# Performance work log

Hardware: AMD Instinct MI355X
Metric: run time of the kernel (lower is better)

Reference implementation:

```python
import jax, jax.numpy as jnp
import numpy as np

MARGIN = 0.3


def _pairwise_dist(x):
    # Exact euclidean cdist; same math as torch.cdist's non-mm mode:
    # sqrt(sum_k (x_i[k]-x_j[k])^2) == sqrt(|x_i|^2 + |x_j|^2 - 2 x_i.x_j).
    sq = jnp.sum(x * x, axis=1)
    sqd = sq[:, None] + sq[None, :] - 2.0 * (x @ x.T)
    sqd = jnp.maximum(sqd, 0.0)
    # safe sqrt: zero distance (diagonal) -> dist 0 with zero grad, like torch
    safe = jnp.where(sqd > 0, sqd, 1.0)
    return jnp.where(sqd > 0, jnp.sqrt(safe), 0.0)


def setup_inputs() -> dict:
    key = jax.random.key(0)
    k1, k2 = jax.random.split(key)
    n, d, n_classes = 8192, 128, 64
    inputs = jax.random.normal(k1, (n, d), dtype=jnp.float32)
    targets = jax.random.randint(k2, (n,), 0, n_classes)
    return {"inputs": inputs, "targets": targets}


def reference(inputs, targets):
    dist = _pairwise_dist(inputs)  # (n, n)
    mask = targets[:, None] == targets[None, :]  # (n, n) same-label mask
    # hard positive: max distance among same-label (diag included, as in torch code)
    dist_ap = jnp.max(jnp.where(mask, dist, -jnp.inf), axis=1)  # (n,)
    # hard negative: min distance among different-label
    dist_an = jnp.min(jnp.where(mask, jnp.inf, dist), axis=1)  # (n,)
    # MarginRankingLoss with y=1: mean(relu(-(dist_an - dist_ap) + margin))
    loss = jnp.mean(jax.nn.relu(dist_ap - dist_an + MARGIN))
    return (loss, dist)
```

## Files before the change

kernel.cpp:

```cpp
#include <hip/hip_runtime.h>
#include <hip/hip_bf16.h>
#include <cstdint>
#include <cstddef>


#define NROWS 8192
#define DIMK  128
#define MARGIN 0.3f

typedef __bf16 bf16x8 __attribute__((ext_vector_type(8)));
typedef float  f32x4  __attribute__((ext_vector_type(4)));
typedef int    i32x4  __attribute__((ext_vector_type(4)));
typedef float  f32x2  __attribute__((ext_vector_type(2)));

__device__ __forceinline__ unsigned short f2bf(float f) {
    unsigned u = __float_as_uint(f);
    u += 0x7fffu + ((u >> 16) & 1u);
    return (unsigned short)(u >> 16);
}

__global__ __launch_bounds__(256) void prep_kernel(
    const float* __restrict__ X, unsigned short* __restrict__ Xb,
    float* __restrict__ sq, int* __restrict__ ap, int* __restrict__ an)
{
    const int t = blockIdx.x * 256 + threadIdx.x;
    if (t < NROWS) { ap[t] = 0; an[t] = 0x7f800000; }
    const int row  = t >> 6;
    const int lane = t & 63;
    const f32x2 v = *(const f32x2*)(X + (size_t)row * DIMK + lane * 2);
    const unsigned short b0 = f2bf(v[0]);
    const unsigned short b1 = f2bf(v[1]);
    *(unsigned*)(Xb + (size_t)row * DIMK + lane * 2) =
        (unsigned)b0 | ((unsigned)b1 << 16);
    const float f0 = __uint_as_float((unsigned)b0 << 16);
    const float f1 = __uint_as_float((unsigned)b1 << 16);
    float s = f0 * f0 + f1 * f1;
    #pragma unroll
    for (int off = 32; off; off >>= 1) s += __shfl_xor(s, off);
    if (lane == 0) sq[row] = s;
}

__global__ __launch_bounds__(256, 2) void dist_kernel(
    const unsigned short* __restrict__ Xb, const float* __restrict__ sq,
    const int* __restrict__ tgt, float* __restrict__ dist,
    int* __restrict__ ap, int* __restrict__ an)
{
    __shared__ unsigned short As[128 * DIMK];
    __shared__ unsigned short Bs[128 * DIMK];

    const int t  = threadIdx.x;
    const int bm = blockIdx.x, bn = blockIdx.y;

    {
        const char* gA = (const char*)Xb + (size_t)bm * (128 * DIMK * 2);
        const char* gB = (const char*)Xb + (size_t)bn * (128 * DIMK * 2);
        #pragma unroll
        for (int i = 0; i < 8; i++) {
            const int off = i * 4096 + t * 16;
            __builtin_amdgcn_global_load_lds(
                (const __attribute__((address_space(1))) void*)(gA + off),
                (__attribute__((address_space(3))) void*)((char*)As + off),
                16, 0, 0);
        }
        #pragma unroll
        for (int i = 0; i < 8; i++) {
            const int off = i * 4096 + t * 16;
            __builtin_amdgcn_global_load_lds(
                (const __attribute__((address_space(1))) void*)(gB + off),
                (__attribute__((address_space(3))) void*)((char*)Bs + off),
                16, 0, 0);
        }
    }
    __syncthreads();

    const int lane = t & 63, wave = t >> 6;
    const int wm = (wave >> 1) * 64, wn = (wave & 1) * 64;
    const int l15 = lane & 15, quad = lane >> 4;

    f32x4 acc[4][4];
    #pragma unroll
    for (int mi = 0; mi < 4; mi++)
        #pragma unroll
        for (int ni = 0; ni < 4; ni++)
            acc[mi][ni] = (f32x4){0.f, 0.f, 0.f, 0.f};

    #pragma unroll
    for (int ks = 0; ks < 4; ks++) {
        const int kb = ks * 32 + quad * 8;
        bf16x8 a_frag[4], b_frag[4];
        #pragma unroll
        for (int mi = 0; mi < 4; mi++)
            a_frag[mi] = *(const bf16x8*)(As + (wm + mi * 16 + l15) * DIMK + kb);
        #pragma unroll
        for (int ni = 0; ni < 4; ni++)
            b_frag[ni] = *(const bf16x8*)(Bs + (wn + ni * 16 + l15) * DIMK + kb);
        #pragma unroll
        for (int mi = 0; mi < 4; mi++)
            #pragma unroll
            for (int ni = 0; ni < 4; ni++)
                acc[mi][ni] = __builtin_amdgcn_mfma_f32_16x16x32_bf16(
                    a_frag[mi], b_frag[ni], acc[mi][ni], 0, 0, 0);
    }

    const int rbase = bm * 128 + wm;
    const int cbase = bn * 128 + wn;
    const float INF = __int_as_float(0x7f800000);

    float sqc[4]; int tc[4]; int cg[4];
    #pragma unroll
    for (int ni = 0; ni < 4; ni++) {
        cg[ni]  = cbase + ni * 16 + l15;
        sqc[ni] = sq[cg[ni]];
        tc[ni]  = tgt[cg[ni]];
    }

    #pragma unroll
    for (int mi = 0; mi < 4; mi++) {
        const int rg0 = rbase + mi * 16 + quad * 4;
        const f32x4 sqr = *(const f32x4*)(sq + rg0);
        const i32x4 tr  = *(const i32x4*)(tgt + rg0);
        #pragma unroll
        for (int reg = 0; reg < 4; reg++) {
            const int rg = rg0 + reg;
            float apv = -1.0f, anv = INF;
            #pragma unroll
            for (int ni = 0; ni < 4; ni++) {
                const float dot = acc[mi][ni][reg];
                float sqd = sqr[reg] + sqc[ni] - 2.0f * dot;
                float d = sqd > 0.0f ? sqrtf(sqd) : 0.0f;
                if (rg == cg[ni]) d = 0.0f;
                __builtin_nontemporal_store(d, dist + (size_t)rg * NROWS + cg[ni]);
                const bool same = (tr[reg] == tc[ni]);
                apv = fmaxf(apv, same ? d : -1.0f);
                anv = fminf(anv, same ? INF : d);
            }
            #pragma unroll
            for (int m = 1; m < 16; m <<= 1) {
                apv = fmaxf(apv, __shfl_xor(apv, m));
                anv = fminf(anv, __shfl_xor(anv, m));
            }
            if (l15 == mi * 4 + reg) {
                atomicMax(ap + rg, __float_as_int(apv));
                atomicMin(an + rg, __float_as_int(anv));
            }
        }
    }
}

__global__ __launch_bounds__(256) void loss_kernel(
    const int* __restrict__ ap, const int* __restrict__ an,
    float* __restrict__ out)
{
    __shared__ float red[4];
    float s = 0.0f;
    for (int i = threadIdx.x; i < NROWS; i += 256) {
        const float v = __int_as_float(ap[i]) - __int_as_float(an[i]) + MARGIN;
        s += v > 0.0f ? v : 0.0f;
    }
    #pragma unroll
    for (int off = 32; off; off >>= 1) s += __shfl_xor(s, off);
    if ((threadIdx.x & 63) == 0) red[threadIdx.x >> 6] = s;
    __syncthreads();
    if (threadIdx.x == 0)
        out[0] = (red[0] + red[1] + red[2] + red[3]) * (1.0f / NROWS);
}

extern "C" void kernel_launch(void* const* d_in, const int* in_sizes, int n_in,
                              void* d_out, int out_size, void* d_ws, size_t ws_size,
                              hipStream_t stream)
{
    const float* X   = (const float*)d_in[0];
    const int*   tgt = (const int*)d_in[1];
    float*       out = (float*)d_out;

    unsigned short* Xb = (unsigned short*)d_ws;
    float* sq = (float*)((char*)d_ws + (size_t)NROWS * DIMK * 2);
    int*   ap = (int*)(sq + NROWS);
    int*   an = ap + NROWS;

    prep_kernel<<<(NROWS * 64) / 256, 256, 0, stream>>>(X, Xb, sq, ap, an);

    dim3 grid(64, 64);
    dist_kernel<<<grid, 256, 0, stream>>>(Xb, sq, tgt, out + 1, ap, an);

    loss_kernel<<<1, 256, 0, stream>>>(ap, an, out);
}
```

Measured before the change: 362.7 us.

## Load MFMA fragments directly from global memory instead of LDS staging

The distance kernel no longer stages the A and B tiles in shared memory with global_load_lds and a barrier. Each wave now reads its bf16 fragments straight from global memory, relying on L1/L2 to serve the reuse, and the occupancy hint rises to three blocks per SM. The final loss reduction moves to a 1024-thread block with a fully unrolled loop and a shuffle-based combine of the per-wave partial sums. This removes LDS usage and the sync, at the cost of redundant global and L2 traffic, since the column tile is re-read by both waves that share it.

Measured after the change: 384.5 us. +6.0%, slower.

```diff
diff --git a/kernel.cpp b/kernel.cpp
--- a/kernel.cpp
+++ b/kernel.cpp
@@ -40,42 +40,20 @@
     if (lane == 0) sq[row] = s;
 }
 
-__global__ __launch_bounds__(256, 2) void dist_kernel(
+__global__ __launch_bounds__(256, 3) void dist_kernel(
     const unsigned short* __restrict__ Xb, const float* __restrict__ sq,
     const int* __restrict__ tgt, float* __restrict__ dist,
     int* __restrict__ ap, int* __restrict__ an)
 {
-    __shared__ unsigned short As[128 * DIMK];
-    __shared__ unsigned short Bs[128 * DIMK];
-
     const int t  = threadIdx.x;
     const int bm = blockIdx.x, bn = blockIdx.y;
-
-    {
-        const char* gA = (const char*)Xb + (size_t)bm * (128 * DIMK * 2);
-        const char* gB = (const char*)Xb + (size_t)bn * (128 * DIMK * 2);
-        #pragma unroll
-        for (int i = 0; i < 8; i++) {
-            const int off = i * 4096 + t * 16;
-            __builtin_amdgcn_global_load_lds(
-                (const __attribute__((address_space(1))) void*)(gA + off),
-                (__attribute__((address_space(3))) void*)((char*)As + off),
-                16, 0, 0);
-        }
-        #pragma unroll
-        for (int i = 0; i < 8; i++) {
-            const int off = i * 4096 + t * 16;
-            __builtin_amdgcn_global_load_lds(
-                (const __attribute__((address_space(1))) void*)(gB + off),
-                (__attribute__((address_space(3))) void*)((char*)Bs + off),
-                16, 0, 0);
-        }
-    }
-    __syncthreads();
 
     const int lane = t & 63, wave = t >> 6;
     const int wm = (wave >> 1) * 64, wn = (wave & 1) * 64;
     const int l15 = lane & 15, quad = lane >> 4;
+
+    const int rbase = bm * 128 + wm;
+    const int cbase = bn * 128 + wn;
 
     f32x4 acc[4][4];
     #pragma unroll
@@ -90,10 +68,10 @@
         bf16x8 a_frag[4], b_frag[4];
         #pragma unroll
         for (int mi = 0; mi < 4; mi++)
-            a_frag[mi] = *(const bf16x8*)(As + (wm + mi * 16 + l15) * DIMK + kb);
+            a_frag[mi] = *(const bf16x8*)(Xb + (size_t)(rbase + mi * 16 + l15) * DIMK + kb);
         #pragma unroll
         for (int ni = 0; ni < 4; ni++)
-            b_frag[ni] = *(const bf16x8*)(Bs + (wn + ni * 16 + l15) * DIMK + kb);
+            b_frag[ni] = *(const bf16x8*)(Xb + (size_t)(cbase + ni * 16 + l15) * DIMK + kb);
         #pragma unroll
         for (int mi = 0; mi < 4; mi++)
             #pragma unroll
@@ -102,8 +80,6 @@
                     a_frag[mi], b_frag[ni], acc[mi][ni], 0, 0, 0);
     }
 
-    const int rbase = bm * 128 + wm;
-    const int cbase = bn * 128 + wn;
     const float INF = __int_as_float(0x7f800000);
 
     float sqc[4]; int tc[4]; int cg[4];
@@ -147,22 +123,28 @@
     }
 }
 
-__global__ __launch_bounds__(256) void loss_kernel(
+__global__ __launch_bounds__(1024) void loss_kernel(
     const int* __restrict__ ap, const int* __restrict__ an,
     float* __restrict__ out)
 {
-    __shared__ float red[4];
+    __shared__ float red[16];
     float s = 0.0f;
-    for (int i = threadIdx.x; i < NROWS; i += 256) {
-        const float v = __int_as_float(ap[i]) - __int_as_float(an[i]) + MARGIN;
+    #pragma unroll
+    for (int i = 0; i < 8; i++) {
+        const int idx = i * 1024 + threadIdx.x;
+        const float v = __int_as_float(ap[idx]) - __int_as_float(an[idx]) + MARGIN;
         s += v > 0.0f ? v : 0.0f;
     }
     #pragma unroll
     for (int off = 32; off; off >>= 1) s += __shfl_xor(s, off);
     if ((threadIdx.x & 63) == 0) red[threadIdx.x >> 6] = s;
     __syncthreads();
-    if (threadIdx.x == 0)
-        out[0] = (red[0] + red[1] + red[2] + red[3]) * (1.0f / NROWS);
+    if (threadIdx.x < 64) {
+        float v = (threadIdx.x < 16) ? red[threadIdx.x] : 0.0f;
+        #pragma unroll
+        for (int off = 8; off; off >>= 1) v += __shfl_xor(v, off);
+        if (threadIdx.x == 0) out[0] = v * (1.0f / NROWS);
+    }
 }
 
 extern "C" void kernel_launch(void* const* d_in, const int* in_sizes, int n_in,
@@ -183,5 +165,5 @@
     dim3 grid(64, 64);
     dist_kernel<<<grid, 256, 0, stream>>>(Xb, sq, tgt, out + 1, ap, an);
 
-    loss_kernel<<<1, 256, 0, stream>>>(ap, an, out);
+    loss_kernel<<<1, 1024, 0, stream>>>(ap, an, out);
 }
```
